# Kernel tuning notes

Measured on AMD Instinct MI355X. Metric: run time of the kernel, lower is better.

The kernel has to match this reference:

```python
import jax, jax.numpy as jnp
import numpy as np

N_NODES = 50000
N_EDGES = 300000
D = 256
N_RELS = 500


def setup_inputs() -> dict:
    key = jax.random.key(0)
    ks = jax.random.split(key, 12)
    s = 1.0 / np.sqrt(D)  # keep activations O(1) through the dense transforms
    return {
        "h": jax.random.normal(ks[0], (N_NODES, D), dtype=jnp.float32),
        "prev_h": jax.random.normal(ks[1], (N_NODES, D), dtype=jnp.float32),
        "emb_rel": jax.random.normal(ks[2], (N_RELS, D), dtype=jnp.float32),
        "norm": jax.random.uniform(ks[3], (N_NODES, 1), dtype=jnp.float32),
        "weight_neighbor": jax.random.normal(ks[4], (D, D), dtype=jnp.float32) * s,
        "loop_weight": jax.random.normal(ks[5], (D, D), dtype=jnp.float32) * s,
        "evolve_loop_weight": jax.random.normal(ks[6], (D, D), dtype=jnp.float32) * s,
        "skip_connect_weight": jax.random.normal(ks[7], (D, D), dtype=jnp.float32) * s,
        "skip_connect_bias": jnp.zeros((D,), dtype=jnp.float32),
        "src": jax.random.randint(ks[8], (N_EDGES,), 0, N_NODES),
        "dst": jax.random.randint(ks[9], (N_EDGES,), 0, N_NODES),
        "etype": jax.random.randint(ks[10], (N_EDGES,), 0, N_RELS),
    }


def reference(h, prev_h, emb_rel, norm, weight_neighbor, loop_weight,
              evolve_loop_weight, skip_connect_weight, skip_connect_bias,
              src, dst, etype):
    n_nodes = h.shape[0]
    # msg_func: per-edge gather of src features + relation embedding, dense transform
    msg = (h[src] + emb_rel[etype]) @ weight_neighbor          # [E, D]
    # fn.sum: segment-sum messages into destination nodes
    agg = jax.ops.segment_sum(msg, dst, num_segments=n_nodes)  # [N, D]
    # apply_func: multiply by per-node norm
    agg = agg * norm
    # self-loop: loop_weight where in_degree > 0, evolve_loop_weight otherwise
    in_deg = jax.ops.segment_sum(jnp.ones_like(dst), dst, num_segments=n_nodes)
    has_in = (in_deg > 0)[:, None]
    loop_message = jnp.where(has_in, h @ loop_weight, h @ evolve_loop_weight)
    # skip connection gate
    skip_weight = jax.nn.sigmoid(prev_h @ skip_connect_weight + skip_connect_bias)
    node_repr = skip_weight * (agg + loop_message) + (1.0 - skip_weight) * prev_h
    return jax.nn.relu(node_repr)
```

## Files before the change

### kernel.cpp

```cpp
#include <hip/hip_runtime.h>
#include <cstdint>
#include <cstddef>

#define N_NODES 50000
#define N_EDGES 300000
#define DIM     256
#define KTOT    768
#define N_RELS  500
#define XW      768

#define SCAN_BLK  256
#define SCAN_NBLK ((N_NODES + SCAN_BLK - 1) / SCAN_BLK)

#define CONV_ELEMS ((2 * N_NODES + N_RELS) * DIM)
#define CONV_BLKS  ((CONV_ELEMS / 8 + 255) / 256)
#define HIST_BLKS  ((N_EDGES + 255) / 256)

typedef unsigned short u16;
typedef __attribute__((ext_vector_type(8))) short short8v;
typedef __attribute__((ext_vector_type(4))) float float4v;

static __device__ __forceinline__ u16 f2bf(float f) {
    union { float f; unsigned u; } v; v.f = f;
    unsigned u = v.u;
    unsigned r = u + 0x7FFFu + ((u >> 16) & 1u);
    return (u16)(r >> 16);
}
static __device__ __forceinline__ float bf2f(u16 b) {
    union { unsigned u; float f; } v; v.u = ((unsigned)b) << 16; return v.f;
}

static __device__ __forceinline__ void gld16(const void* g, u16* l) {
    __builtin_amdgcn_global_load_lds(
        (const __attribute__((address_space(1))) unsigned int*)g,
        (__attribute__((address_space(3))) unsigned int*)l,
        16, 0, 0);
}

__global__ void prep_kernel(const float* __restrict__ h, const float* __restrict__ prev_h,
                            const float* __restrict__ emb,
                            const float* __restrict__ Wn, const float* __restrict__ Wl,
                            const float* __restrict__ Wsc, const int* __restrict__ dstv,
                            u16* __restrict__ Xcat, u16* __restrict__ embb,
                            u16* __restrict__ Wt, int* __restrict__ deg) {
    int b = blockIdx.x;
    if (b < CONV_BLKS) {
        int i = b * 256 + threadIdx.x;
        int e0 = i * 8;
        if (e0 >= CONV_ELEMS) return;
        const float* s; u16* d;
        if (e0 < N_NODES * DIM) {
            int n = e0 >> 8, c = e0 & 255;
            s = h + e0; d = Xcat + (size_t)n * XW + 256 + c;
        } else if (e0 < 2 * N_NODES * DIM) {
            int o = e0 - N_NODES * DIM;
            int n = o >> 8, c = o & 255;
            s = prev_h + o; d = Xcat + (size_t)n * XW + 512 + c;
        } else {
            int o = e0 - 2 * N_NODES * DIM;
            s = emb + o; d = embb + o;
        }
        float4 a = *(const float4*)(s);
        float4 c2 = *(const float4*)(s + 4);
        u16 o8[8] = { f2bf(a.x), f2bf(a.y), f2bf(a.z), f2bf(a.w),
                      f2bf(c2.x), f2bf(c2.y), f2bf(c2.z), f2bf(c2.w) };
        *(uint4*)d = *(const uint4*)o8;
    } else if (b < CONV_BLKS + KTOT) {
        int k = b - CONV_BLKS;
        int dd = threadIdx.x;
        const float* W = (k < 256) ? Wn : ((k < 512) ? Wl : Wsc);
        Wt[(size_t)dd * KTOT + k] = f2bf(W[(k & 255) * DIM + dd]);
    } else {
        int e = (b - CONV_BLKS - KTOT) * 256 + threadIdx.x;
        if (e < N_EDGES) atomicAdd(&deg[dstv[e]], 1);
    }
}

__global__ void scanA_kernel(const int* __restrict__ deg, int* __restrict__ excl_local,
                             int* __restrict__ block_sum) {
    __shared__ int sdata[SCAN_BLK];
    int t = threadIdx.x, i = blockIdx.x * SCAN_BLK + t;
    int v = (i < N_NODES) ? deg[i] : 0;
    sdata[t] = v;
    __syncthreads();
    for (int off = 1; off < SCAN_BLK; off <<= 1) {
        int u = (t >= off) ? sdata[t - off] : 0;
        __syncthreads();
        sdata[t] += u;
        __syncthreads();
    }
    if (i < N_NODES) excl_local[i] = sdata[t] - v;
    if (t == SCAN_BLK - 1) block_sum[blockIdx.x] = sdata[t];
}

__global__ void scanB_kernel(const int* __restrict__ block_sum, int* __restrict__ block_base,
                             int* __restrict__ offsets) {
    __shared__ int sdata[SCAN_NBLK];
    int t = threadIdx.x;
    int v = (t < SCAN_NBLK) ? block_sum[t] : 0;
    if (t < SCAN_NBLK) sdata[t] = v;
    __syncthreads();
    for (int off = 1; off < SCAN_NBLK; off <<= 1) {
        int u = (t >= off && t < SCAN_NBLK) ? sdata[t - off] : 0;
        __syncthreads();
        if (t < SCAN_NBLK) sdata[t] += u;
        __syncthreads();
    }
    if (t < SCAN_NBLK) block_base[t] = sdata[t] - v;
    if (t == SCAN_NBLK - 1) offsets[N_NODES] = sdata[t];
}

__global__ void scanC_kernel(const int* __restrict__ excl_local, const int* __restrict__ block_base,
                             int* __restrict__ offsets, int* __restrict__ cursor) {
    int i = blockIdx.x * SCAN_BLK + threadIdx.x;
    if (i < N_NODES) {
        int e = block_base[blockIdx.x] + excl_local[i];
        offsets[i] = e; cursor[i] = e;
    }
}

__global__ void scatter_kernel(const int* __restrict__ src, const int* __restrict__ dstv,
                               const int* __restrict__ et, int* __restrict__ cursor,
                               unsigned* __restrict__ esee) {
    int e = blockIdx.x * 256 + threadIdx.x;
    if (e >= N_EDGES) return;
    int d = dstv[e];
    int pos = atomicAdd(&cursor[d], 1);
    esee[pos] = (unsigned)src[e] * N_RELS + (unsigned)et[e];
}

__global__ void agg_kernel(u16* __restrict__ Xcat, const u16* __restrict__ embb,
                           const float* __restrict__ norm, const int* __restrict__ offsets,
                           const unsigned* __restrict__ esee,
                           int* __restrict__ wl_count, int* __restrict__ wl) {
    int wave = (blockIdx.x * 256 + threadIdx.x) >> 6;
    int lane = threadIdx.x & 63;
    if (wave >= N_NODES) return;
    int n = wave;
    int s0 = offsets[n], s1 = offsets[n + 1];
    int c4 = lane * 4;
    float4 acc = make_float4(0.f, 0.f, 0.f, 0.f);
    int e = s0;
    for (; e + 3 < s1; e += 4) {
        unsigned v0 = esee[e], v1 = esee[e + 1], v2 = esee[e + 2], v3 = esee[e + 3];
        unsigned sa = v0 / N_RELS, ta = v0 - sa * N_RELS;
        unsigned sb = v1 / N_RELS, tb = v1 - sb * N_RELS;
        unsigned sc = v2 / N_RELS, tc = v2 - sc * N_RELS;
        unsigned sd = v3 / N_RELS, td = v3 - sd * N_RELS;
        ushort4 ha = *(const ushort4*)(Xcat + (size_t)sa * XW + 256 + c4);
        ushort4 ea = *(const ushort4*)(embb + (size_t)ta * DIM + c4);
        ushort4 hb = *(const ushort4*)(Xcat + (size_t)sb * XW + 256 + c4);
        ushort4 eb = *(const ushort4*)(embb + (size_t)tb * DIM + c4);
        ushort4 hc = *(const ushort4*)(Xcat + (size_t)sc * XW + 256 + c4);
        ushort4 ec = *(const ushort4*)(embb + (size_t)tc * DIM + c4);
        ushort4 hd = *(const ushort4*)(Xcat + (size_t)sd * XW + 256 + c4);
        ushort4 ed = *(const ushort4*)(embb + (size_t)td * DIM + c4);
        acc.x += (bf2f(ha.x) + bf2f(ea.x)) + (bf2f(hb.x) + bf2f(eb.x))
               + (bf2f(hc.x) + bf2f(ec.x)) + (bf2f(hd.x) + bf2f(ed.x));
        acc.y += (bf2f(ha.y) + bf2f(ea.y)) + (bf2f(hb.y) + bf2f(eb.y))
               + (bf2f(hc.y) + bf2f(ec.y)) + (bf2f(hd.y) + bf2f(ed.y));
        acc.z += (bf2f(ha.z) + bf2f(ea.z)) + (bf2f(hb.z) + bf2f(eb.z))
               + (bf2f(hc.z) + bf2f(ec.z)) + (bf2f(hd.z) + bf2f(ed.z));
        acc.w += (bf2f(ha.w) + bf2f(ea.w)) + (bf2f(hb.w) + bf2f(eb.w))
               + (bf2f(hc.w) + bf2f(ec.w)) + (bf2f(hd.w) + bf2f(ed.w));
    }
    for (; e < s1; e++) {
        unsigned v = esee[e];
        unsigned s = v / N_RELS;
        unsigned t = v - s * N_RELS;
        ushort4 hv = *(const ushort4*)(Xcat + (size_t)s * XW + 256 + c4);
        ushort4 ev = *(const ushort4*)(embb + (size_t)t * DIM + c4);
        acc.x += bf2f(hv.x) + bf2f(ev.x);
        acc.y += bf2f(hv.y) + bf2f(ev.y);
        acc.z += bf2f(hv.z) + bf2f(ev.z);
        acc.w += bf2f(hv.w) + bf2f(ev.w);
    }
    float nr = norm[n];
    u16 o[4] = { f2bf(acc.x * nr), f2bf(acc.y * nr), f2bf(acc.z * nr), f2bf(acc.w * nr) };
    *(ushort4*)(Xcat + (size_t)n * XW + c4) = *(const ushort4*)o;
    if (lane == 0 && s1 == s0) { int idx = atomicAdd(wl_count, 1); wl[idx] = n; }
}

__launch_bounds__(256, 2)
__global__ void gemm_kernel(const u16* __restrict__ Xcat, const u16* __restrict__ Wt,
                            const float* __restrict__ prev_h, const float* __restrict__ bias,
                            float* __restrict__ out) {
    __shared__ __align__(16) u16 lds[40960];
    int tid  = threadIdx.x;
    int wave = tid >> 6, lane = tid & 63, q = lane >> 4, m16 = lane & 15;
    int wn = wave * 64;
    int m0 = blockIdx.x * 64;
    int lr = lane >> 3, lc8 = lane & 7;
    int scol = (lc8 ^ lr) << 3;

    int ar0 = wave * 16 + lr, ar1 = ar0 + 8;
    int ga0 = (m0 + ar0 < N_NODES) ? (m0 + ar0) : (N_NODES - 1);
    int ga1 = (m0 + ar1 < N_NODES) ? (m0 + ar1) : (N_NODES - 1);
    const u16* sA0 = Xcat + (size_t)ga0 * XW + scol;
    const u16* sA1 = Xcat + (size_t)ga1 * XW + scol;
    const u16* sB  = Wt + (size_t)(wave * 64 + lr) * KTOT + scol;
    int ldsA_w = wave * 16 * 64;
    int ldsB_w = 8192 + wave * 64 * 64;

    float4v acc1[4][4], acc2[4][4];
#pragma unroll
    for (int i = 0; i < 4; i++)
#pragma unroll
        for (int j = 0; j < 4; j++) { acc1[i][j] = (float4v)0.f; acc2[i][j] = (float4v)0.f; }

    auto stage = [&](int kt, int buf) {
#pragma unroll
        for (int j = 0; j < 8; j++)
            gld16(sB + (size_t)j * 8 * KTOT + kt * 64, &lds[ldsB_w + buf * 16384 + j * 512]);
        gld16(sA0 + kt * 64, &lds[ldsA_w + buf * 4096]);
        gld16(sA1 + kt * 64, &lds[ldsA_w + buf * 4096 + 512]);
    };

    stage(0, 0);
    stage(1, 1);

    int sw = (m16 & 7) << 3;

#pragma unroll
    for (int kt = 0; kt < 12; kt++) {
        int buf = kt & 1;
        if (kt < 11) asm volatile("s_waitcnt vmcnt(10)" ::: "memory");
        else         asm volatile("s_waitcnt vmcnt(0)"  ::: "memory");
        __builtin_amdgcn_sched_barrier(0);
        __builtin_amdgcn_s_barrier();
        __builtin_amdgcn_sched_barrier(0);

#pragma unroll
        for (int kk = 0; kk < 2; kk++) {
            int ck = (kk * 32 + q * 8) ^ sw;
            short8v af[4], bfr[4];
#pragma unroll
            for (int mi = 0; mi < 4; mi++)
                af[mi] = *(const short8v*)(&lds[buf * 4096 + (mi * 16 + m16) * 64 + ck]);
#pragma unroll
            for (int ni = 0; ni < 4; ni++)
                bfr[ni] = *(const short8v*)(&lds[8192 + buf * 16384 + (wn + ni * 16 + m16) * 64 + ck]);
            if (kt < 8) {
#pragma unroll
                for (int mi = 0; mi < 4; mi++)
#pragma unroll
                    for (int ni = 0; ni < 4; ni++)
                        acc1[mi][ni] = __builtin_amdgcn_mfma_f32_16x16x32_bf16(
                            af[mi], bfr[ni], acc1[mi][ni], 0, 0, 0);
            } else {
#pragma unroll
                for (int mi = 0; mi < 4; mi++)
#pragma unroll
                    for (int ni = 0; ni < 4; ni++)
                        acc2[mi][ni] = __builtin_amdgcn_mfma_f32_16x16x32_bf16(
                            af[mi], bfr[ni], acc2[mi][ni], 0, 0, 0);
            }
        }

        __builtin_amdgcn_sched_barrier(0);
        __builtin_amdgcn_s_barrier();
        __builtin_amdgcn_sched_barrier(0);
        if (kt + 2 < 12) stage(kt + 2, buf);
    }

#pragma unroll
    for (int mi = 0; mi < 4; mi++) {
#pragma unroll
        for (int ni = 0; ni < 4; ni++) {
            int d = wn + ni * 16 + m16;
            float b = bias[d];
#pragma unroll
            for (int r = 0; r < 4; r++) {
                int node = m0 + mi * 16 + q * 4 + r;
                if (node < N_NODES) {
                    float S  = acc2[mi][ni][r] + b;
                    float sg = 1.f / (1.f + __expf(-S));
                    float ph = prev_h[(size_t)node * DIM + d];
                    float v  = sg * acc1[mi][ni][r] + (1.f - sg) * ph;
                    out[(size_t)node * DIM + d] = fmaxf(v, 0.f);
                }
            }
        }
    }
}

__global__ void fixup_kernel(const float* __restrict__ h, const float* __restrict__ prev_h,
                             const float* __restrict__ We, const float* __restrict__ Wsc,
                             const float* __restrict__ bias, const int* __restrict__ wl_count,
                             const int* __restrict__ wl, float* __restrict__ out) {
    __shared__ float ph[DIM], hh[DIM];
    int d = threadIdx.x;
    int cnt = *wl_count;
    for (int i = blockIdx.x; i < cnt; i += gridDim.x) {
        int n = wl[i];
        ph[d] = prev_h[(size_t)n * DIM + d];
        hh[d] = h[(size_t)n * DIM + d];
        __syncthreads();
        float s = 0.f, l = 0.f;
        for (int k = 0; k < DIM; k++) {
            s += ph[k] * Wsc[k * DIM + d];
            l += hh[k] * We[k * DIM + d];
        }
        float sg = 1.f / (1.f + __expf(-(s + bias[d])));
        float v = sg * l + (1.f - sg) * ph[d];
        out[(size_t)n * DIM + d] = fmaxf(v, 0.f);
        __syncthreads();
    }
}

extern "C" void kernel_launch(void* const* d_in, const int* in_sizes, int n_in,
                              void* d_out, int out_size, void* d_ws, size_t ws_size,
                              hipStream_t stream) {
    const float* h      = (const float*)d_in[0];
    const float* prev_h = (const float*)d_in[1];
    const float* emb    = (const float*)d_in[2];
    const float* norm   = (const float*)d_in[3];
    const float* Wn     = (const float*)d_in[4];
    const float* Wl     = (const float*)d_in[5];
    const float* We     = (const float*)d_in[6];
    const float* Wsc    = (const float*)d_in[7];
    const float* bias   = (const float*)d_in[8];
    const int*   src    = (const int*)d_in[9];
    const int*   dstv   = (const int*)d_in[10];
    const int*   et     = (const int*)d_in[11];
    float* out = (float*)d_out;

    char* ws = (char*)d_ws;
    size_t off = 0;
    auto alloc = [&](size_t bytes) -> char* {
        char* p = ws + off; off += (bytes + 255) & ~(size_t)255; return p;
    };
    u16* Xcat    = (u16*)alloc((size_t)N_NODES * XW * 2);
    u16* embb    = (u16*)alloc((size_t)N_RELS * DIM * 2);
    u16* Wt      = (u16*)alloc((size_t)DIM * KTOT * 2);
    int* deg     = (int*)alloc((size_t)N_NODES * 4);
    int* wlcnt   = (int*)alloc(16);
    int* wl      = (int*)alloc((size_t)N_NODES * 4);
    int* offsets = (int*)alloc((size_t)(N_NODES + 1) * 4);
    int* cursor  = (int*)alloc((size_t)N_NODES * 4);
    unsigned* esee = (unsigned*)alloc((size_t)N_EDGES * 4);
    int* excl    = (int*)alloc((size_t)N_NODES * 4);
    int* bsum    = (int*)alloc((size_t)SCAN_NBLK * 4);
    int* bbase   = (int*)alloc((size_t)SCAN_NBLK * 4);

    hipMemsetAsync(deg, 0, (size_t)N_NODES * 4, stream);
    hipMemsetAsync(wlcnt, 0, 4, stream);

    prep_kernel<<<CONV_BLKS + KTOT + HIST_BLKS, 256, 0, stream>>>(
        h, prev_h, emb, Wn, Wl, Wsc, dstv, Xcat, embb, Wt, deg);
    scanA_kernel<<<SCAN_NBLK, SCAN_BLK, 0, stream>>>(deg, excl, bsum);
    scanB_kernel<<<1, SCAN_BLK, 0, stream>>>(bsum, bbase, offsets);
    scanC_kernel<<<SCAN_NBLK, SCAN_BLK, 0, stream>>>(excl, bbase, offsets, cursor);
    scatter_kernel<<<(N_EDGES + 255) / 256, 256, 0, stream>>>(src, dstv, et, cursor, esee);
    agg_kernel<<<(N_NODES + 3) / 4, 256, 0, stream>>>(Xcat, embb, norm, offsets, esee, wlcnt, wl);
    gemm_kernel<<<(N_NODES + 63) / 64, 256, 0, stream>>>(Xcat, Wt, prev_h, bias, out);
    fixup_kernel<<<256, 256, 0, stream>>>(h, prev_h, We, Wsc, bias, wlcnt, wl, out);
}
```

Measured before the change: 319.0 us.

## Stage GEMM A tiles through registers instead of direct global-to-LDS loads

Result: slower. 334.8 us (+4.9%).

```diff
diff --git a/kernel.cpp b/kernel.cpp
--- a/kernel.cpp
+++ b/kernel.cpp
@@ -199,8 +199,9 @@
     const u16* sA0 = Xcat + (size_t)ga0 * XW + scol;
     const u16* sA1 = Xcat + (size_t)ga1 * XW + scol;
     const u16* sB  = Wt + (size_t)(wave * 64 + lr) * KTOT + scol;
-    int ldsA_w = wave * 16 * 64;
     int ldsB_w = 8192 + wave * 64 * 64;
+    int ldsA_t0 = wave * 16 * 64 + lane * 8;
+    int ldsA_t1 = ldsA_t0 + 512;
 
     float4v acc1[4][4], acc2[4][4];
 #pragma unroll
@@ -208,27 +209,35 @@
 #pragma unroll
         for (int j = 0; j < 4; j++) { acc1[i][j] = (float4v)0.f; acc2[i][j] = (float4v)0.f; }
 
-    auto stage = [&](int kt, int buf) {
+    uint4 rA[2][2];
+
+    auto loadA = [&](int kt, int s) {
+        rA[s][0] = *(const uint4*)(sA0 + kt * 64);
+        rA[s][1] = *(const uint4*)(sA1 + kt * 64);
+    };
+    auto writeA = [&](int buf, int s) {
+        *(uint4*)(&lds[buf * 4096 + ldsA_t0]) = rA[s][0];
+        *(uint4*)(&lds[buf * 4096 + ldsA_t1]) = rA[s][1];
+    };
+    auto stageB = [&](int kt, int buf) {
 #pragma unroll
         for (int j = 0; j < 8; j++)
             gld16(sB + (size_t)j * 8 * KTOT + kt * 64, &lds[ldsB_w + buf * 16384 + j * 512]);
-        gld16(sA0 + kt * 64, &lds[ldsA_w + buf * 4096]);
-        gld16(sA1 + kt * 64, &lds[ldsA_w + buf * 4096 + 512]);
     };
 
-    stage(0, 0);
-    stage(1, 1);
+    loadA(0, 0);
+    loadA(1, 1);
+    stageB(0, 0);
+    writeA(0, 0);
+    __syncthreads();
 
     int sw = (m16 & 7) << 3;
 
 #pragma unroll
     for (int kt = 0; kt < 12; kt++) {
-        int buf = kt & 1;
-        if (kt < 11) asm volatile("s_waitcnt vmcnt(10)" ::: "memory");
-        else         asm volatile("s_waitcnt vmcnt(0)"  ::: "memory");
-        __builtin_amdgcn_sched_barrier(0);
-        __builtin_amdgcn_s_barrier();
-        __builtin_amdgcn_sched_barrier(0);
+        int buf = kt & 1, nbuf = buf ^ 1;
+        if (kt + 1 < 12) stageB(kt + 1, nbuf);
+        if (kt + 2 < 12) loadA(kt + 2, kt & 1);
 
 #pragma unroll
         for (int kk = 0; kk < 2; kk++) {
@@ -257,10 +266,8 @@
             }
         }
 
-        __builtin_amdgcn_sched_barrier(0);
-        __builtin_amdgcn_s_barrier();
-        __builtin_amdgcn_sched_barrier(0);
-        if (kt + 2 < 12) stage(kt + 2, buf);
+        if (kt + 1 < 12) writeA(nbuf, (kt + 1) & 1);
+        __syncthreads();
     }
 
 #pragma unroll
```
